# Kernel optimization log

Measured on AMD Instinct MI355X. Metric: run time of the kernel, lower is better.

Reference implementation:

```python
import jax, jax.numpy as jnp
import numpy as np

B, T = 2048, 8192


def setup_inputs() -> dict:
    key = jax.random.key(0)
    k1, k2, k3, k4 = jax.random.split(key, 4)
    return {
        "target_angle": jax.random.normal(k1, (B, T), dtype=jnp.float32),
        "target_class": jax.random.normal(k2, (B, 3), dtype=jnp.float32),
        "pred_angle": jax.random.normal(k3, (B, T), dtype=jnp.float32),
        "pred_class": jax.random.normal(k4, (B, 3), dtype=jnp.float32),
    }


def reference(target_angle, target_class, pred_angle, pred_class):
    # score_angle: WMA(target) - WMA(pred) == WMA(target - pred) since WMA is linear.
    # Padding 2 zeros per side + 5-tap valid correlation yields T output positions,
    # exactly matching the original python loop over range(T+4-4).
    w = jnp.asarray([0.05, 0.1, 0.7, 0.1, 0.05], dtype=target_angle.dtype)
    diff = target_angle - pred_angle                       # [B, T]
    dp = jnp.pad(diff, ((0, 0), (2, 2)))                   # [B, T+4]
    t = diff.shape[1]
    # 5-term fused sum instead of per-position slice loop
    wma = (w[0] * dp[:, 0:t] + w[1] * dp[:, 1:t + 1] + w[2] * dp[:, 2:t + 2]
           + w[3] * dp[:, 3:t + 3] + w[4] * dp[:, 4:t + 4])  # [B, T]
    d_angle = jnp.sum(wma * wma)

    # score_class: sum of squared errors over the first 3 class columns
    dc = target_class[:, :3] - pred_class[:, :3]
    d_class = jnp.sum(dc * dc)

    return d_angle * 0.8 + d_class * 0.2
```

## Files before the change

kernel.cpp:

```cpp
#include <hip/hip_runtime.h>


#define NTHREADS 256
#define PER_THREAD 8

typedef float f32x4 __attribute__((ext_vector_type(4)));

__global__ __launch_bounds__(NTHREADS) void wma_partial_kernel(
    const float* __restrict__ ta, const float* __restrict__ pa,
    float* __restrict__ partial, int T)
{
    const int t = threadIdx.x;
    const long e = ((long)blockIdx.x * NTHREADS + t) * PER_THREAD;
    const int col = (int)(e % T);

    const f32x4* ta4 = (const f32x4*)(ta + e);
    const f32x4* pa4 = (const f32x4*)(pa + e);
    const f32x4 a0 = __builtin_nontemporal_load(ta4);
    const f32x4 a1 = __builtin_nontemporal_load(ta4 + 1);
    const f32x4 p0 = __builtin_nontemporal_load(pa4);
    const f32x4 p1 = __builtin_nontemporal_load(pa4 + 1);

    const float d0 = a0.x - p0.x, d1 = a0.y - p0.y, d2 = a0.z - p0.z, d3 = a0.w - p0.w;
    const float d4 = a1.x - p1.x, d5 = a1.y - p1.y, d6 = a1.z - p1.z, d7 = a1.w - p1.w;

    const int lane = t & 63;
    float dm2 = __shfl_up(d6, 1, 64);
    float dm1 = __shfl_up(d7, 1, 64);
    float dp8 = __shfl_down(d0, 1, 64);
    float dp9 = __shfl_down(d1, 1, 64);

    if (lane == 0) {
        dm1 = (col >= 1) ? (ta[e - 1] - pa[e - 1]) : 0.0f;
        dm2 = (col >= 2) ? (ta[e - 2] - pa[e - 2]) : 0.0f;
    }
    if (lane == 63) {
        dp8 = (col + PER_THREAD     < T) ? (ta[e + 8] - pa[e + 8]) : 0.0f;
        dp9 = (col + PER_THREAD + 1 < T) ? (ta[e + 9] - pa[e + 9]) : 0.0f;
    }

    float acc = 0.0f, w;
    w = 0.05f*dm2 + 0.1f*dm1 + 0.7f*d0 + 0.1f*d1  + 0.05f*d2;  acc += w*w;
    w = 0.05f*dm1 + 0.1f*d0  + 0.7f*d1 + 0.1f*d2  + 0.05f*d3;  acc += w*w;
    w = 0.05f*d0  + 0.1f*d1  + 0.7f*d2 + 0.1f*d3  + 0.05f*d4;  acc += w*w;
    w = 0.05f*d1  + 0.1f*d2  + 0.7f*d3 + 0.1f*d4  + 0.05f*d5;  acc += w*w;
    w = 0.05f*d2  + 0.1f*d3  + 0.7f*d4 + 0.1f*d5  + 0.05f*d6;  acc += w*w;
    w = 0.05f*d3  + 0.1f*d4  + 0.7f*d5 + 0.1f*d6  + 0.05f*d7;  acc += w*w;
    w = 0.05f*d4  + 0.1f*d5  + 0.7f*d6 + 0.1f*d7  + 0.05f*dp8; acc += w*w;
    w = 0.05f*d5  + 0.1f*d6  + 0.7f*d7 + 0.1f*dp8 + 0.05f*dp9; acc += w*w;

#pragma unroll
    for (int off = 32; off; off >>= 1) acc += __shfl_down(acc, off, 64);

    __shared__ float wsum[NTHREADS / 64];
    if ((t & 63) == 0) wsum[t >> 6] = acc;
    __syncthreads();
    if (t == 0) {
        float b = 0.0f;
#pragma unroll
        for (int i = 0; i < NTHREADS / 64; ++i) b += wsum[i];
        partial[blockIdx.x] = b;
    }
}

#define FIN_THREADS 1024

__global__ __launch_bounds__(FIN_THREADS) void finalize_kernel(
    const float* __restrict__ partial, int nPartial,
    const float* __restrict__ tc, const float* __restrict__ pc, int nClass,
    float* __restrict__ out)
{
    const int t = threadIdx.x;

    float sa = 0.0f;
    for (int i = t; i < nPartial; i += FIN_THREADS) sa += partial[i];

    float sc = 0.0f;
    for (int i = t; i < nClass; i += FIN_THREADS) {
        const float d = tc[i] - pc[i];
        sc += d * d;
    }

#pragma unroll
    for (int off = 32; off; off >>= 1) {
        sa += __shfl_down(sa, off, 64);
        sc += __shfl_down(sc, off, 64);
    }

    __shared__ float ra[FIN_THREADS / 64], rc[FIN_THREADS / 64];
    if ((t & 63) == 0) { ra[t >> 6] = sa; rc[t >> 6] = sc; }
    __syncthreads();
    if (t == 0) {
        float a = 0.0f, c = 0.0f;
#pragma unroll
        for (int i = 0; i < FIN_THREADS / 64; ++i) { a += ra[i]; c += rc[i]; }
        out[0] = 0.8f * a + 0.2f * c;
    }
}

extern "C" void kernel_launch(void* const* d_in, const int* in_sizes, int n_in,
                              void* d_out, int out_size, void* d_ws, size_t ws_size,
                              hipStream_t stream)
{
    const float* ta = (const float*)d_in[0];
    const float* tc = (const float*)d_in[1];
    const float* pa = (const float*)d_in[2];
    const float* pc = (const float*)d_in[3];
    float* out = (float*)d_out;

    const int nAngle = in_sizes[0];
    const int nClass = in_sizes[1];
    const int T = 8192;
    const int grid = nAngle / (NTHREADS * PER_THREAD);

    float* partial = (float*)d_ws;

    wma_partial_kernel<<<grid, NTHREADS, 0, stream>>>(ta, pa, partial, T);
    finalize_kernel<<<1, FIN_THREADS, 0, stream>>>(partial, grid, tc, pc, nClass, out);
}
```

Measured before the change: 38.04 us.

## Process multiple strided chunks per thread with a depth-4 register prefetch pipeline

Each thread now handles eight 8-element chunks spaced one grid-span apart, instead of a single chunk. Loads are issued four chunks ahead into register buffers so several memory requests stay in flight while earlier chunks are reduced. The grid shrinks by a factor of eight, which also cuts the number of partial sums the finalize kernel must add. In exchange the kernel uses more registers, may run at lower occupancy, and relies on the span being a multiple of T so the edge handling per column stays valid.

Measured after the change: 41.16 us. 8.2% more time.

```diff
diff --git a/kernel.cpp b/kernel.cpp
--- a/kernel.cpp
+++ b/kernel.cpp
@@ -2,7 +2,8 @@
 
 
 #define NTHREADS 256
-#define PER_THREAD 8
+#define ITERS 8
+#define DEPTH 4
 
 typedef float f32x4 __attribute__((ext_vector_type(4)));
 
@@ -11,43 +12,66 @@
     float* __restrict__ partial, int T)
 {
     const int t = threadIdx.x;
-    const long e = ((long)blockIdx.x * NTHREADS + t) * PER_THREAD;
-    const int col = (int)(e % T);
+    const int lane = t & 63;
+    const long span = (long)gridDim.x * NTHREADS * 8;
+    const long base = ((long)blockIdx.x * NTHREADS + t) * 8;
+    const int col = (int)(base % T);
+    const bool edge0  = (lane == 0)  && (col > 0);
+    const bool edge63 = (lane == 63) && (col + 8 < T);
 
-    const f32x4* ta4 = (const f32x4*)(ta + e);
-    const f32x4* pa4 = (const f32x4*)(pa + e);
-    const f32x4 a0 = __builtin_nontemporal_load(ta4);
-    const f32x4 a1 = __builtin_nontemporal_load(ta4 + 1);
-    const f32x4 p0 = __builtin_nontemporal_load(pa4);
-    const f32x4 p1 = __builtin_nontemporal_load(pa4 + 1);
+    f32x4 A[DEPTH][2], P[DEPTH][2];
+    float em1[DEPTH], em2[DEPTH], ep8[DEPTH], ep9[DEPTH];
 
-    const float d0 = a0.x - p0.x, d1 = a0.y - p0.y, d2 = a0.z - p0.z, d3 = a0.w - p0.w;
-    const float d4 = a1.x - p1.x, d5 = a1.y - p1.y, d6 = a1.z - p1.z, d7 = a1.w - p1.w;
+#define ISSUE(c) do {                                                     \
+        const int s_ = (c) & (DEPTH - 1);                                 \
+        const long e_ = base + (long)(c) * span;                          \
+        const f32x4* tap_ = (const f32x4*)(ta + e_);                      \
+        const f32x4* pap_ = (const f32x4*)(pa + e_);                      \
+        A[s_][0] = __builtin_nontemporal_load(tap_);                      \
+        A[s_][1] = __builtin_nontemporal_load(tap_ + 1);                  \
+        P[s_][0] = __builtin_nontemporal_load(pap_);                      \
+        P[s_][1] = __builtin_nontemporal_load(pap_ + 1);                  \
+        em1[s_] = edge0  ? ta[e_ - 1] - pa[e_ - 1] : 0.0f;                \
+        em2[s_] = edge0  ? ta[e_ - 2] - pa[e_ - 2] : 0.0f;                \
+        ep8[s_] = edge63 ? ta[e_ + 8] - pa[e_ + 8] : 0.0f;                \
+        ep9[s_] = edge63 ? ta[e_ + 9] - pa[e_ + 9] : 0.0f;                \
+    } while (0)
 
-    const int lane = t & 63;
-    float dm2 = __shfl_up(d6, 1, 64);
-    float dm1 = __shfl_up(d7, 1, 64);
-    float dp8 = __shfl_down(d0, 1, 64);
-    float dp9 = __shfl_down(d1, 1, 64);
+    ISSUE(0); ISSUE(1); ISSUE(2); ISSUE(3);
 
-    if (lane == 0) {
-        dm1 = (col >= 1) ? (ta[e - 1] - pa[e - 1]) : 0.0f;
-        dm2 = (col >= 2) ? (ta[e - 2] - pa[e - 2]) : 0.0f;
+    float acc = 0.0f;
+#pragma unroll
+    for (int c = 0; c < ITERS; ++c) {
+        const int s = c & (DEPTH - 1);
+        const float d0 = A[s][0].x - P[s][0].x;
+        const float d1 = A[s][0].y - P[s][0].y;
+        const float d2 = A[s][0].z - P[s][0].z;
+        const float d3 = A[s][0].w - P[s][0].w;
+        const float d4 = A[s][1].x - P[s][1].x;
+        const float d5 = A[s][1].y - P[s][1].y;
+        const float d6 = A[s][1].z - P[s][1].z;
+        const float d7 = A[s][1].w - P[s][1].w;
+
+        float dm2 = __shfl_up(d6, 1, 64);
+        float dm1 = __shfl_up(d7, 1, 64);
+        float dp8 = __shfl_down(d0, 1, 64);
+        float dp9 = __shfl_down(d1, 1, 64);
+        if (lane == 0)  { dm2 = em2[s]; dm1 = em1[s]; }
+        if (lane == 63) { dp8 = ep8[s]; dp9 = ep9[s]; }
+
+        float w;
+        w = 0.05f*dm2 + 0.1f*dm1 + 0.7f*d0 + 0.1f*d1  + 0.05f*d2;  acc += w*w;
+        w = 0.05f*dm1 + 0.1f*d0  + 0.7f*d1 + 0.1f*d2  + 0.05f*d3;  acc += w*w;
+        w = 0.05f*d0  + 0.1f*d1  + 0.7f*d2 + 0.1f*d3  + 0.05f*d4;  acc += w*w;
+        w = 0.05f*d1  + 0.1f*d2  + 0.7f*d3 + 0.1f*d4  + 0.05f*d5;  acc += w*w;
+        w = 0.05f*d2  + 0.1f*d3  + 0.7f*d4 + 0.1f*d5  + 0.05f*d6;  acc += w*w;
+        w = 0.05f*d3  + 0.1f*d4  + 0.7f*d5 + 0.1f*d6  + 0.05f*d7;  acc += w*w;
+        w = 0.05f*d4  + 0.1f*d5  + 0.7f*d6 + 0.1f*d7  + 0.05f*dp8; acc += w*w;
+        w = 0.05f*d5  + 0.1f*d6  + 0.7f*d7 + 0.1f*dp8 + 0.05f*dp9; acc += w*w;
+
+        if (c + DEPTH < ITERS) ISSUE(c + DEPTH);
     }
-    if (lane == 63) {
-        dp8 = (col + PER_THREAD     < T) ? (ta[e + 8] - pa[e + 8]) : 0.0f;
-        dp9 = (col + PER_THREAD + 1 < T) ? (ta[e + 9] - pa[e + 9]) : 0.0f;
-    }
-
-    float acc = 0.0f, w;
-    w = 0.05f*dm2 + 0.1f*dm1 + 0.7f*d0 + 0.1f*d1  + 0.05f*d2;  acc += w*w;
-    w = 0.05f*dm1 + 0.1f*d0  + 0.7f*d1 + 0.1f*d2  + 0.05f*d3;  acc += w*w;
-    w = 0.05f*d0  + 0.1f*d1  + 0.7f*d2 + 0.1f*d3  + 0.05f*d4;  acc += w*w;
-    w = 0.05f*d1  + 0.1f*d2  + 0.7f*d3 + 0.1f*d4  + 0.05f*d5;  acc += w*w;
-    w = 0.05f*d2  + 0.1f*d3  + 0.7f*d4 + 0.1f*d5  + 0.05f*d6;  acc += w*w;
-    w = 0.05f*d3  + 0.1f*d4  + 0.7f*d5 + 0.1f*d6  + 0.05f*d7;  acc += w*w;
-    w = 0.05f*d4  + 0.1f*d5  + 0.7f*d6 + 0.1f*d7  + 0.05f*dp8; acc += w*w;
-    w = 0.05f*d5  + 0.1f*d6  + 0.7f*d7 + 0.1f*dp8 + 0.05f*dp9; acc += w*w;
+#undef ISSUE
 
 #pragma unroll
     for (int off = 32; off; off >>= 1) acc += __shfl_down(acc, off, 64);
@@ -111,7 +135,7 @@
     const int nAngle = in_sizes[0];
     const int nClass = in_sizes[1];
     const int T = 8192;
-    const int grid = nAngle / (NTHREADS * PER_THREAD);
+    const int grid = nAngle / (NTHREADS * 8 * ITERS);
 
     float* partial = (float*)d_ws;
 
```
